# Optimization experiments

Measured on AMD Instinct MI355X. Metric: run time of the kernel, lower is better.

The kernel has to match this reference:

```python
import jax, jax.numpy as jnp
import numpy as np

B, LT, D, H, DI = 8, 128, 512, 8, 2048
NMEM, LMEM = 1024, 64
DH = D // H
EPS = 1e-5
NEG = -1e9

def _ln(x, g, b):
    mu = x.mean(-1, keepdims=True)
    var = ((x - mu) ** 2).mean(-1, keepdims=True)
    return (x - mu) * jax.lax.rsqrt(var + EPS) * g + b

def _ffn(x, W1, b1, W2, b2):
    # PositionwiseFF with residual=True (dropout=0 / eval)
    return x + jax.nn.relu(x @ W1 + b1) @ W2 + b2

def setup_inputs():
    key = jax.random.key(0)
    ks = jax.random.split(key, 16)
    w = lambda i, shape: jax.random.normal(ks[i], shape, jnp.float32) * 0.02
    return {
        "dec_output": jax.random.normal(ks[0], (B, LT, D), jnp.float32),
        "mem_attn_out": jax.random.normal(ks[1], (B, LT, NMEM + 1), jnp.float32),
        "enc_out_mem": jax.random.normal(ks[2], (NMEM, LMEM, D), jnp.float32),
        "tgt_emb_mem": jax.random.normal(ks[3], (NMEM, LMEM, D), jnp.float32),
        "tgt_mask_mem": jax.random.randint(ks[4], (NMEM, LMEM), 0, 2, jnp.int32),
        "tgt_mask": jax.random.randint(ks[5], (B, LT), 0, 2, jnp.int32),
        "g0": jnp.ones((D,), jnp.float32), "be0": jnp.zeros((D,), jnp.float32),
        "g1": jnp.ones((D,), jnp.float32), "be1": jnp.zeros((D,), jnp.float32),
        "Wq": w(6, (D, D)), "bq": jnp.zeros((D,), jnp.float32),
        "Wk": w(7, (D, D)), "bk": jnp.zeros((D,), jnp.float32),
        "Wv": w(8, (D, D)), "bv": jnp.zeros((D,), jnp.float32),
        "Wo": w(9, (D, D)), "bo": jnp.zeros((D,), jnp.float32),
        "f1W1": w(10, (D, DI)), "f1b1": jnp.zeros((DI,), jnp.float32),
        "f1W2": w(11, (DI, D)), "f1b2": jnp.zeros((D,), jnp.float32),
        "f2W1": w(12, (D, DI)), "f2b1": jnp.zeros((DI,), jnp.float32),
        "f2W2": w(13, (DI, D)), "f2b2": jnp.zeros((D,), jnp.float32),
    }

def reference(dec_output, mem_attn_out, enc_out_mem, tgt_emb_mem, tgt_mask_mem, tgt_mask,
              g0, be0, g1, be1, Wq, bq, Wk, bk, Wv, bv, Wo, bo,
              f1W1, f1b1, f1W2, f1b2, f2W1, f2b1, f2W2, f2b2):
    x = _ln(dec_output, g0, be0)                       # [B,LT,D]
    N = B * LT
    samples = jnp.argmax(mem_attn_out, -1).reshape(N) - 1   # [-1, NMEM-1]
    valid = samples >= 0                               # [N]
    s = jnp.maximum(samples, 0)                        # clamp; masked later
    q = x.reshape(N, 1, D)
    # gather memory per selected query (torch compacts via unique; same math)
    k_in = enc_out_mem[s]                              # [N,LMEM,D]
    v_in = tgt_emb_mem[s]                              # [N,LMEM,D]
    kmask = tgt_mask_mem[s] != 0                       # True = valid key
    # multi-head attention, residual=True
    qh = (q @ Wq + bq).reshape(N, 1, H, DH).transpose(0, 2, 1, 3)     # [N,H,1,DH]
    kh = (k_in @ Wk + bk).reshape(N, LMEM, H, DH).transpose(0, 2, 1, 3)
    vh = (v_in @ Wv + bv).reshape(N, LMEM, H, DH).transpose(0, 2, 1, 3)
    scores = jnp.einsum('nhqd,nhkd->nhqk', qh, kh) / (DH ** 0.5)      # [N,H,1,LMEM]
    scores = jnp.where(kmask[:, None, None, :], scores, NEG)
    attn = jax.nn.softmax(scores, axis=-1)
    ctx = jnp.einsum('nhqk,nhkd->nhqd', attn, vh).transpose(0, 2, 1, 3).reshape(N, 1, D)
    st = q + ctx @ Wo + bo
    st = _ffn(st, f1W1, f1b1, f1W2, f1b2)
    st = _ln(st, g1, be1)
    # scatter back: positions with sample == -1 get zeros
    st = jnp.where(valid[:, None, None], st, 0.0)
    dec = x + st.reshape(B, LT, D)
    dec = _ffn(dec, f2W1, f2b1, f2W2, f2b2)
    return dec
```

## Files before the change

kernel.cpp:

```cpp
#include <hip/hip_runtime.h>
#include <math.h>

#define NQ   1024
#define DIM  512
#define NH   8
#define DHD  64
#define DFF  2048
#define LM   64

typedef __bf16 bf16x8 __attribute__((ext_vector_type(8)));
typedef float  f32x4  __attribute__((ext_vector_type(4)));

__device__ __forceinline__ unsigned short f2bf(float f) {
    unsigned u = __builtin_bit_cast(unsigned, f);
    return (unsigned short)((u + 0x7fffu + ((u >> 16) & 1u)) >> 16);
}
__device__ __forceinline__ float bflo(unsigned p) {
    return __builtin_bit_cast(float, p << 16);
}
__device__ __forceinline__ float bfhi(unsigned p) {
    return __builtin_bit_cast(float, p & 0xffff0000u);
}

__device__ __forceinline__ void gload16(const void* g, void* l) {
    __builtin_amdgcn_global_load_lds(
        (const __attribute__((address_space(1))) unsigned*)g,
        (__attribute__((address_space(3))) unsigned*)l, 16, 0, 0);
}

__device__ __forceinline__ float blk_sum(float v, volatile float* red) {
#pragma unroll
    for (int o = 32; o; o >>= 1) v += __shfl_down(v, o);
    __syncthreads();
    if ((threadIdx.x & 63) == 0) red[threadIdx.x >> 6] = v;
    __syncthreads();
    return red[0] + red[1] + red[2] + red[3];
}

__global__ __launch_bounds__(256) void ln0_argmax_k(
    const float* __restrict__ dec_out, const float* __restrict__ attn_out,
    const float* __restrict__ g, const float* __restrict__ be,
    float* __restrict__ x, unsigned* __restrict__ xb, int* __restrict__ samples)
{
    __shared__ float red[4];
    __shared__ float rv[4]; __shared__ int ri[4];
    const int n = blockIdx.x, t = threadIdx.x;

    float2 v = ((const float2*)(dec_out + (size_t)n * DIM))[t];
    float mu  = blk_sum(v.x + v.y, red) * (1.f / DIM);
    float dx = v.x - mu, dy = v.y - mu;
    float var = blk_sum(dx * dx + dy * dy, red) * (1.f / DIM);
    float rs = rsqrtf(var + 1e-5f);
    float2 gg = ((const float2*)g)[t], bb = ((const float2*)be)[t];
    float ox = dx * rs * gg.x + bb.x, oy = dy * rs * gg.y + bb.y;
    ((float2*)(x + (size_t)n * DIM))[t] = make_float2(ox, oy);
    xb[(size_t)n * 256 + t] = (unsigned)f2bf(ox) | ((unsigned)f2bf(oy) << 16);

    const float* ar = attn_out + (size_t)n * 1025;
    float bv = -INFINITY; int bi = 0x7fffffff;
    for (int i = t; i < 1025; i += 256) {
        float val = ar[i];
        if (val > bv || (val == bv && i < bi)) { bv = val; bi = i; }
    }
#pragma unroll
    for (int o = 32; o; o >>= 1) {
        float ov = __shfl_down(bv, o); int oi = __shfl_down(bi, o);
        if (ov > bv || (ov == bv && oi < bi)) { bv = ov; bi = oi; }
    }
    if ((t & 63) == 0) { rv[t >> 6] = bv; ri[t >> 6] = bi; }
    __syncthreads();
    if (t == 0) {
#pragma unroll
        for (int w = 1; w < 4; ++w)
            if (rv[w] > bv || (rv[w] == bv && ri[w] < bi)) { bv = rv[w]; bi = ri[w]; }
        samples[n] = bi - 1;
    }
}

struct PrepPtrs {
    const float* src[8];
    unsigned short* dst[8];
};
__global__ __launch_bounds__(256) void prep_weights_k(PrepPtrs p) {
    __shared__ float tile[32][33];
    const int bid = blockIdx.x;
    int m, lt;
    if (bid < 1024) { m = bid >> 8; lt = bid & 255; }
    else { m = 4 + ((bid - 1024) >> 10); lt = (bid - 1024) & 1023; }
    const int RS = (m < 4) ? 512 : ((m == 5 || m == 7) ? 2048 : 512);
    const int CS = (m < 4) ? 512 : ((m == 5 || m == 7) ? 512 : 2048);
    const int TC = CS >> 5;
    const int tr = lt / TC, tc = lt % TC;
    const float* s = p.src[m];
    unsigned short* d = p.dst[m];
    const int tx = threadIdx.x & 31, ty = threadIdx.x >> 5;
    if (m == 1) {
#pragma unroll
        for (int i = 0; i < 32; i += 8) {
            size_t idx = (size_t)(tr * 32 + ty + i) * CS + tc * 32 + tx;
            d[idx] = f2bf(s[idx]);
        }
    } else {
#pragma unroll
        for (int i = 0; i < 32; i += 8)
            tile[ty + i][tx] = s[(size_t)(tr * 32 + ty + i) * CS + tc * 32 + tx];
        __syncthreads();
#pragma unroll
        for (int i = 0; i < 32; i += 8)
            d[(size_t)(tc * 32 + ty + i) * RS + tr * 32 + tx] = f2bf(tile[tx][ty + i]);
    }
}

template<bool RELU, bool BIAS, bool RES, bool WF32, bool WBF>
__global__ __launch_bounds__(256) void mfma_gemm(
    const unsigned short* __restrict__ A, const unsigned short* __restrict__ Bt,
    float* __restrict__ Cf, unsigned short* __restrict__ Cb,
    const float* __restrict__ bias, const float* __restrict__ res,
    int K, int lda, int ldb, int ldc,
    int sA, int sB, int sC, int sBias)
{
    __shared__ unsigned short Ab[2][64 * 64];
    __shared__ unsigned short Bb[2][64 * 64];
    const int t = threadIdx.x, lane = t & 63, wid = t >> 6;
    const int bm = blockIdx.y * 64, bn = blockIdx.x * 64, bz = blockIdx.z;
    const unsigned short* Abase = A + (size_t)bz * sA + (size_t)bm * lda;
    const unsigned short* Bbase = Bt + (size_t)bz * sB + (size_t)bn * ldb;

    const int r0 = wid * 16 + (lane >> 3);
    const int cbs = lane & 7;

#define STAGE_T(buf, base, ld, kt)                                              \
    {                                                                           \
        int r_ = r0;                                                            \
        gload16(base + (size_t)r_ * ld + (kt) * 64 + ((cbs ^ (r_ & 7)) << 3),   \
                &buf[(wid * 2 + 0) * 512]);                                     \
        r_ = r0 + 8;                                                            \
        gload16(base + (size_t)r_ * ld + (kt) * 64 + ((cbs ^ (r_ & 7)) << 3),   \
                &buf[(wid * 2 + 1) * 512]);                                     \
    }

    const int lr = lane & 15, lg = lane >> 4;
    const int wr = (wid >> 1) * 32, wc = (wid & 1) * 32;
    const int mA0 = wr + lr, mA1 = wr + 16 + lr;
    const int nB0 = wc + lr, nB1 = wc + 16 + lr;
    f32x4 acc[2][2] = {};

#define COMPUTE(b)                                                              \
    _Pragma("unroll")                                                           \
    for (int kk = 0; kk < 2; ++kk) {                                            \
        const int kb = kk * 4 + lg;                                             \
        bf16x8 a0 = *(const bf16x8*)&Ab[b][mA0 * 64 + ((kb ^ (mA0 & 7)) << 3)]; \
        bf16x8 a1 = *(const bf16x8*)&Ab[b][mA1 * 64 + ((kb ^ (mA1 & 7)) << 3)]; \
        bf16x8 b0 = *(const bf16x8*)&Bb[b][nB0 * 64 + ((kb ^ (nB0 & 7)) << 3)]; \
        bf16x8 b1 = *(const bf16x8*)&Bb[b][nB1 * 64 + ((kb ^ (nB1 & 7)) << 3)]; \
        acc[0][0] = __builtin_amdgcn_mfma_f32_16x16x32_bf16(a0, b0, acc[0][0], 0, 0, 0); \
        acc[0][1] = __builtin_amdgcn_mfma_f32_16x16x32_bf16(a0, b1, acc[0][1], 0, 0, 0); \
        acc[1][0] = __builtin_amdgcn_mfma_f32_16x16x32_bf16(a1, b0, acc[1][0], 0, 0, 0); \
        acc[1][1] = __builtin_amdgcn_mfma_f32_16x16x32_bf16(a1, b1, acc[1][1], 0, 0, 0); \
    }

    STAGE_T(Ab[0], Abase, lda, 0);
    STAGE_T(Bb[0], Bbase, ldb, 0);
    __syncthreads();
    const int NT = K >> 6;
    int cur = 0;
    for (int kt = 0; kt < NT; ++kt) {
        if (kt + 1 < NT) {
            STAGE_T(Ab[cur ^ 1], Abase, lda, kt + 1);
            STAGE_T(Bb[cur ^ 1], Bbase, ldb, kt + 1);
        }
        if (cur == 0) { COMPUTE(0); } else { COMPUTE(1); }
        __syncthreads();
        cur ^= 1;
    }

#pragma unroll
    for (int fm = 0; fm < 2; ++fm)
#pragma unroll
    for (int fn = 0; fn < 2; ++fn) {
        const int col = bn + wc + fn * 16 + lr;
        float bia = BIAS ? bias[bz * sBias + col] : 0.f;
#pragma unroll
        for (int r = 0; r < 4; ++r) {
            const int row = bm + wr + fm * 16 + lg * 4 + r;
            const size_t ci = (size_t)bz * sC + (size_t)row * ldc + col;
            float v = acc[fm][fn][r] + bia;
            if (RES) v += res[(size_t)row * ldc + col];
            if (RELU) v = fmaxf(v, 0.f);
            if (WF32) Cf[ci] = v;
            if (WBF)  Cb[ci] = f2bf(v);
        }
    }
#undef STAGE_T
#undef COMPUTE
}

__global__ __launch_bounds__(256) void attn_mem_k(
    const float* __restrict__ qh, const unsigned short* __restrict__ u_bf,
    const float* __restrict__ enc, const float* __restrict__ vemb,
    const int* __restrict__ maskmem, const int* __restrict__ samples,
    const float* __restrict__ bk, unsigned* __restrict__ a_bf)
{
    __shared__ alignas(16) unsigned short U_lds[16 * 512];
    __shared__ float S_lds[8 * 68];
    __shared__ alignas(16) unsigned short P_lds[64 * 8];
    __shared__ float Cs_lds[8];
    __shared__ int Msk_lds[64];

    const int n = blockIdx.x, t = threadIdx.x;
    const int lane = t & 63, w = t >> 6;
    int s = samples[n]; if (s < 0) s = 0;

    {
        const uint4* ub = (const uint4*)(u_bf + (size_t)n * 4096);
#pragma unroll
        for (int i = 0; i < 4; ++i) {
            int chunk = t + i * 256;
            int h = chunk >> 6, c8 = chunk & 63;
            uint4 v = (h < 8) ? ub[chunk] : make_uint4(0, 0, 0, 0);
            *(uint4*)&U_lds[h * 512 + (c8 ^ (h & 7)) * 8] = v;
        }
        if (w == 0) Msk_lds[lane] = maskmem[(size_t)s * LM + lane];
        if (w == 1) {
            int h = lane >> 3, j = lane & 7;
            const float4* q4 = (const float4*)(qh + (size_t)n * DIM + h * 64 + j * 8);
            const float4* b4 = (const float4*)(bk + h * 64 + j * 8);
            float4 qa = q4[0], qb = q4[1], ba = b4[0], bb = b4[1];
            float c = qa.x * ba.x + qa.y * ba.y + qa.z * ba.z + qa.w * ba.w
                    + qb.x * bb.x + qb.y * bb.y + qb.z * bb.z + qb.w * bb.w;
            c += __shfl_xor(c, 1); c += __shfl_xor(c, 2); c += __shfl_xor(c, 4);
            if (j == 0) Cs_lds[h] = c;
        }
    }
    __syncthreads();

    {
        const float4* kb = (const float4*)(enc + (size_t)s * (LM * DIM));
        const int key = w * 16 + (lane & 15);
        const int lg = lane >> 4;
        const int h = lane & 15;
        const int base = key * 128 + lg * 2;
        f32x4 acc = {};
        float4 pf[4][2];
#pragma unroll
        for (int ss = 0; ss < 4; ++ss) {
            pf[ss][0] = kb[base + ss * 8];
            pf[ss][1] = kb[base + ss * 8 + 1];
        }
#pragma unroll
        for (int step = 0; step < 16; ++step) {
            float4 a0 = pf[step & 3][0], a1 = pf[step & 3][1];
            if (step + 4 < 16) {
                pf[step & 3][0] = kb[base + (step + 4) * 8];
                pf[step & 3][1] = kb[base + (step + 4) * 8 + 1];
            }
            bf16x8 af;
            af[0] = (__bf16)a0.x; af[1] = (__bf16)a0.y;
            af[2] = (__bf16)a0.z; af[3] = (__bf16)a0.w;
            af[4] = (__bf16)a1.x; af[5] = (__bf16)a1.y;
            af[6] = (__bf16)a1.z; af[7] = (__bf16)a1.w;
            const int c8 = step * 4 + lg;
            bf16x8 bfr = *(const bf16x8*)&U_lds[h * 512 + (c8 ^ (h & 7)) * 8];
            acc = __builtin_amdgcn_mfma_f32_16x16x32_bf16(af, bfr, acc, 0, 0, 0);
        }
        if (h < 8) {
#pragma unroll
            for (int r = 0; r < 4; ++r)
                S_lds[h * 68 + w * 16 + lg * 4 + r] = acc[r];
        }
    }
    __syncthreads();

#pragma unroll
    for (int hh = 0; hh < 2; ++hh) {
        const int h = w + hh * 4;
        float sc = (S_lds[h * 68 + lane] + Cs_lds[h]) * 0.125f;
        sc = (Msk_lds[lane] != 0) ? sc : -1e9f;
        float m = sc;
#pragma unroll
        for (int o = 32; o; o >>= 1) m = fmaxf(m, __shfl_xor(m, o));
        float e = __expf(sc - m);
        float su = e;
#pragma unroll
        for (int o = 32; o; o >>= 1) su += __shfl_xor(su, o);
        P_lds[lane * 8 + h] = f2bf(e / su);
    }
    __syncthreads();

    {
        float2 acc8[8];
#pragma unroll
        for (int h = 0; h < 8; ++h) acc8[h] = make_float2(0.f, 0.f);
        const float2* vb = (const float2*)(vemb + (size_t)s * (LM * DIM)) + t;
#pragma unroll 8
        for (int k = 0; k < 64; ++k) {
            float2 v = vb[k * 256];
            uint4 pr = *(const uint4*)&P_lds[k * 8];
            float p0 = bflo(pr.x), p1 = bfhi(pr.x);
            float p2 = bflo(pr.y), p3 = bfhi(pr.y);
            float p4 = bflo(pr.z), p5 = bfhi(pr.z);
            float p6 = bflo(pr.w), p7 = bfhi(pr.w);
            acc8[0].x = fmaf(p0, v.x, acc8[0].x); acc8[0].y = fmaf(p0, v.y, acc8[0].y);
            acc8[1].x = fmaf(p1, v.x, acc8[1].x); acc8[1].y = fmaf(p1, v.y, acc8[1].y);
            acc8[2].x = fmaf(p2, v.x, acc8[2].x); acc8[2].y = fmaf(p2, v.y, acc8[2].y);
            acc8[3].x = fmaf(p3, v.x, acc8[3].x); acc8[3].y = fmaf(p3, v.y, acc8[3].y);
            acc8[4].x = fmaf(p4, v.x, acc8[4].x); acc8[4].y = fmaf(p4, v.y, acc8[4].y);
            acc8[5].x = fmaf(p5, v.x, acc8[5].x); acc8[5].y = fmaf(p5, v.y, acc8[5].y);
            acc8[6].x = fmaf(p6, v.x, acc8[6].x); acc8[6].y = fmaf(p6, v.y, acc8[6].y);
            acc8[7].x = fmaf(p7, v.x, acc8[7].x); acc8[7].y = fmaf(p7, v.y, acc8[7].y);
        }
        unsigned* an = a_bf + (size_t)n * 2048;
#pragma unroll
        for (int h = 0; h < 8; ++h)
            an[h * 256 + t] = (unsigned)f2bf(acc8[h].x) | ((unsigned)f2bf(acc8[h].y) << 16);
    }
}

__global__ __launch_bounds__(256) void ln1_mask_add_k(
    const float* __restrict__ t1, const float* __restrict__ g,
    const float* __restrict__ be, const int* __restrict__ samples,
    const float* __restrict__ x, float* __restrict__ dec, unsigned* __restrict__ decb)
{
    __shared__ float red[4];
    const int n = blockIdx.x, t = threadIdx.x;
    float2 v = ((const float2*)(t1 + (size_t)n * DIM))[t];
    float mu  = blk_sum(v.x + v.y, red) * (1.f / DIM);
    float dx = v.x - mu, dy = v.y - mu;
    float var = blk_sum(dx * dx + dy * dy, red) * (1.f / DIM);
    float rs = rsqrtf(var + 1e-5f);
    float2 gg = ((const float2*)g)[t], bb = ((const float2*)be)[t];
    float sx = dx * rs * gg.x + bb.x, sy = dy * rs * gg.y + bb.y;
    if (samples[n] < 0) { sx = 0.f; sy = 0.f; }
    float2 xx = ((const float2*)(x + (size_t)n * DIM))[t];
    float ox = xx.x + sx, oy = xx.y + sy;
    ((float2*)(dec + (size_t)n * DIM))[t] = make_float2(ox, oy);
    decb[(size_t)n * 256 + t] = (unsigned)f2bf(ox) | ((unsigned)f2bf(oy) << 16);
}

extern "C" void kernel_launch(void* const* d_in, const int* in_sizes, int n_in,
                              void* d_out, int out_size, void* d_ws, size_t ws_size,
                              hipStream_t stream)
{
    const float* dec_output = (const float*)d_in[0];
    const float* mem_attn   = (const float*)d_in[1];
    const float* enc_mem    = (const float*)d_in[2];
    const float* temb_mem   = (const float*)d_in[3];
    const int*   mask_mem   = (const int*)d_in[4];
    const float* g0  = (const float*)d_in[6];
    const float* be0 = (const float*)d_in[7];
    const float* g1  = (const float*)d_in[8];
    const float* be1 = (const float*)d_in[9];
    const float* Wq  = (const float*)d_in[10];
    const float* bq  = (const float*)d_in[11];
    const float* Wk  = (const float*)d_in[12];
    const float* bk  = (const float*)d_in[13];
    const float* Wv  = (const float*)d_in[14];
    const float* bv  = (const float*)d_in[15];
    const float* Wo  = (const float*)d_in[16];
    const float* bo  = (const float*)d_in[17];
    const float* f1W1 = (const float*)d_in[18];
    const float* f1b1 = (const float*)d_in[19];
    const float* f1W2 = (const float*)d_in[20];
    const float* f1b2 = (const float*)d_in[21];
    const float* f2W1 = (const float*)d_in[22];
    const float* f2b1 = (const float*)d_in[23];
    const float* f2W2 = (const float*)d_in[24];
    const float* f2b2 = (const float*)d_in[25];
    float* out = (float*)d_out;

    float* ws = (float*)d_ws;
    float*          x_f   = ws + 0;
    unsigned*       x_b   = (unsigned*)(ws + 524288);
    float*          qh_f  = ws + 786432;
    unsigned short* qh_b  = (unsigned short*)(ws + 1310720);
    unsigned short* u_b   = (unsigned short*)(ws + 1572864);
    unsigned short* a_b   = (unsigned short*)(ws + 3670016);
    unsigned short* wqt   = (unsigned short*)(ws + 5767168);
    unsigned short* wkc   = (unsigned short*)(ws + 5898240);
    unsigned short* wvt   = (unsigned short*)(ws + 6029312);
    unsigned short* wot   = (unsigned short*)(ws + 6160384);
    unsigned short* f1w1t = (unsigned short*)(ws + 6291456);
    unsigned short* f1w2t = (unsigned short*)(ws + 6815744);
    unsigned short* f2w1t = (unsigned short*)(ws + 7340032);
    unsigned short* f2w2t = (unsigned short*)(ws + 7864320);
    int*            smp   = (int*)(ws + 8388608);
    float*          st0_f = (float*)u_b + 0;
    unsigned short* st0_b = (unsigned short*)((float*)u_b + 524288);
    float*          t1_f  = (float*)u_b + 786432;
    float*          dec_f = (float*)u_b + 1310720;
    unsigned*       dec_b = (unsigned*)((float*)u_b + 1835008);
    unsigned short* h1_b  = a_b;
    unsigned short* h2_b  = (unsigned short*)((float*)a_b + 1048576);

    PrepPtrs pp;
    pp.src[0] = Wq;   pp.dst[0] = wqt;
    pp.src[1] = Wk;   pp.dst[1] = wkc;
    pp.src[2] = Wv;   pp.dst[2] = wvt;
    pp.src[3] = Wo;   pp.dst[3] = wot;
    pp.src[4] = f1W1; pp.dst[4] = f1w1t;
    pp.src[5] = f1W2; pp.dst[5] = f1w2t;
    pp.src[6] = f2W1; pp.dst[6] = f2w1t;
    pp.src[7] = f2W2; pp.dst[7] = f2w2t;
    prep_weights_k<<<5120, 256, 0, stream>>>(pp);
    ln0_argmax_k<<<NQ, 256, 0, stream>>>(dec_output, mem_attn, g0, be0, x_f, x_b, smp);
    mfma_gemm<false, true, false, true, true><<<dim3(8, 16, 1), 256, 0, stream>>>(
        (const unsigned short*)x_b, wqt, qh_f, qh_b, bq, nullptr,
        DIM, DIM, DIM, DIM, 0, 0, 0, 0);
    mfma_gemm<false, false, false, false, true><<<dim3(8, 16, NH), 256, 0, stream>>>(
        qh_b, wkc, nullptr, u_b, nullptr, nullptr,
        DHD, DIM, DIM, NH * DIM, DHD, DHD, DIM, 0);
    attn_mem_k<<<NQ, 256, 0, stream>>>(qh_f, u_b, enc_mem, temb_mem, mask_mem, smp,
                                       bk, (unsigned*)a_b);
    mfma_gemm<false, true, false, false, true><<<dim3(1, 16, NH), 256, 0, stream>>>(
        a_b, wvt, nullptr, qh_b, bv, nullptr,
        DIM, NH * DIM, DIM, DIM, DIM, DHD * DIM, DHD, DHD);
    mfma_gemm<false, true, true, true, true><<<dim3(8, 16, 1), 256, 0, stream>>>(
        qh_b, wot, st0_f, st0_b, bo, x_f, DIM, DIM, DIM, DIM, 0, 0, 0, 0);
    mfma_gemm<true, true, false, false, true><<<dim3(32, 16, 1), 256, 0, stream>>>(
        st0_b, f1w1t, nullptr, h1_b, f1b1, nullptr, DIM, DIM, DIM, DFF, 0, 0, 0, 0);
    mfma_gemm<false, true, true, true, false><<<dim3(8, 16, 1), 256, 0, stream>>>(
        h1_b, f1w2t, t1_f, nullptr, f1b2, st0_f, DFF, DFF, DFF, DIM, 0, 0, 0, 0);
    ln1_mask_add_k<<<NQ, 256, 0, stream>>>(t1_f, g1, be1, smp, x_f, dec_f, dec_b);
    mfma_gemm<true, true, false, false, true><<<dim3(32, 16, 1), 256, 0, stream>>>(
        (const unsigned short*)dec_b, f2w1t, nullptr, h2_b, f2b1, nullptr,
        DIM, DIM, DIM, DFF, 0, 0, 0, 0);
    mfma_gemm<false, true, true, true, false><<<dim3(8, 16, 1), 256, 0, stream>>>(
        h2_b, f2w2t, out, nullptr, f2b2, dec_f, DFF, DFF, DFF, DIM, 0, 0, 0, 0);

    (void)in_sizes; (void)n_in; (void)out_size; (void)ws_size;
}
```

Baseline: 162.7 us.

## Split memory attention into scores and PV kernels; add 128x128 FFN up-projection GEMM

The fused memory-attention kernel is split into a scores/softmax kernel and a separate P·V kernel. The scores kernel reads the projected query fragments straight from global memory instead of staging them in LDS. The P·V kernel runs two blocks per query, each covering half the columns, with the key range split across half-blocks and reduced through LDS, which doubles parallelism. A new double-buffered 128x128-tile MFMA GEMM replaces the generic GEMM for both FFN first layers, raising per-block data reuse at the cost of fewer blocks (128) and more registers.

Measured after the change: 172.7 us. +6.2%, slower.

```diff
diff --git a/kernel.cpp b/kernel.cpp
--- a/kernel.cpp
+++ b/kernel.cpp
@@ -195,15 +195,98 @@
 #undef COMPUTE
 }
 
-__global__ __launch_bounds__(256) void attn_mem_k(
+template<bool RELU>
+__global__ __launch_bounds__(256) void mfma_gemm128(
+    const unsigned short* __restrict__ A, const unsigned short* __restrict__ Bt,
+    unsigned short* __restrict__ Cb, const float* __restrict__ bias,
+    int K, int lda, int ldb, int ldc)
+{
+    __shared__ unsigned short Ab[2][128 * 64];
+    __shared__ unsigned short Bb[2][128 * 64];
+    const int t = threadIdx.x, lane = t & 63, wid = t >> 6;
+    const int bn = blockIdx.x * 128, bm = blockIdx.y * 128;
+    const unsigned short* Abase = A + (size_t)bm * lda;
+    const unsigned short* Bbase = Bt + (size_t)bn * ldb;
+
+    const int srow = lane >> 3;
+    const int c8 = lane & 7;
+
+#define STAGE128(buf, base, ld, kt)                                             \
+    _Pragma("unroll")                                                           \
+    for (int i = 0; i < 4; ++i) {                                               \
+        int row = i * 32 + wid * 8 + srow;                                      \
+        gload16(base + (size_t)row * ld + (kt) * 64 + ((c8 ^ (row & 7)) << 3),  \
+                &buf[(i * 32 + wid * 8) * 64]);                                 \
+    }
+
+    const int lr = lane & 15, lg = lane >> 4;
+    const int wr = (wid >> 1) * 64, wc = (wid & 1) * 64;
+    f32x4 acc[4][4] = {};
+
+#define COMPUTE128(b)                                                           \
+    _Pragma("unroll")                                                           \
+    for (int kk = 0; kk < 2; ++kk) {                                            \
+        const int kb = kk * 4 + lg;                                             \
+        bf16x8 af[4], bfv[4];                                                   \
+        _Pragma("unroll")                                                       \
+        for (int fm = 0; fm < 4; ++fm) {                                        \
+            int row = wr + fm * 16 + lr;                                        \
+            af[fm] = *(const bf16x8*)&Ab[b][row * 64 + ((kb ^ (row & 7)) << 3)];\
+        }                                                                       \
+        _Pragma("unroll")                                                       \
+        for (int fn = 0; fn < 4; ++fn) {                                        \
+            int col = wc + fn * 16 + lr;                                        \
+            bfv[fn] = *(const bf16x8*)&Bb[b][col * 64 + ((kb ^ (col & 7)) << 3)];\
+        }                                                                       \
+        _Pragma("unroll")                                                       \
+        for (int fm = 0; fm < 4; ++fm)                                          \
+            _Pragma("unroll")                                                   \
+            for (int fn = 0; fn < 4; ++fn)                                      \
+                acc[fm][fn] = __builtin_amdgcn_mfma_f32_16x16x32_bf16(          \
+                    af[fm], bfv[fn], acc[fm][fn], 0, 0, 0);                     \
+    }
+
+    STAGE128(Ab[0], Abase, lda, 0);
+    STAGE128(Bb[0], Bbase, ldb, 0);
+    __syncthreads();
+    const int NT = K >> 6;
+    int cur = 0;
+    for (int kt = 0; kt < NT; ++kt) {
+        if (kt + 1 < NT) {
+            STAGE128(Ab[cur ^ 1], Abase, lda, kt + 1);
+            STAGE128(Bb[cur ^ 1], Bbase, ldb, kt + 1);
+        }
+        if (cur == 0) { COMPUTE128(0); } else { COMPUTE128(1); }
+        __syncthreads();
+        cur ^= 1;
+    }
+
+#pragma unroll
+    for (int fn = 0; fn < 4; ++fn) {
+        const int col = bn + wc + fn * 16 + lr;
+        const float bia = bias[col];
+#pragma unroll
+        for (int fm = 0; fm < 4; ++fm) {
+#pragma unroll
+            for (int r = 0; r < 4; ++r) {
+                const int row = bm + wr + fm * 16 + lg * 4 + r;
+                float v = acc[fm][fn][r] + bia;
+                if (RELU) v = fmaxf(v, 0.f);
+                Cb[(size_t)row * ldc + col] = f2bf(v);
+            }
+        }
+    }
+#undef STAGE128
+#undef COMPUTE128
+}
+
+__global__ __launch_bounds__(256) void attn_scores_k(
     const float* __restrict__ qh, const unsigned short* __restrict__ u_bf,
-    const float* __restrict__ enc, const float* __restrict__ vemb,
-    const int* __restrict__ maskmem, const int* __restrict__ samples,
-    const float* __restrict__ bk, unsigned* __restrict__ a_bf)
-{
-    __shared__ alignas(16) unsigned short U_lds[16 * 512];
+    const float* __restrict__ enc, const int* __restrict__ maskmem,
+    const int* __restrict__ samples, const float* __restrict__ bk,
+    unsigned short* __restrict__ p_out)
+{
     __shared__ float S_lds[8 * 68];
-    __shared__ alignas(16) unsigned short P_lds[64 * 8];
     __shared__ float Cs_lds[8];
     __shared__ int Msk_lds[64];
 
@@ -211,70 +294,59 @@
     const int lane = t & 63, w = t >> 6;
     int s = samples[n]; if (s < 0) s = 0;
 
-    {
-        const uint4* ub = (const uint4*)(u_bf + (size_t)n * 4096);
-#pragma unroll
-        for (int i = 0; i < 4; ++i) {
-            int chunk = t + i * 256;
-            int h = chunk >> 6, c8 = chunk & 63;
-            uint4 v = (h < 8) ? ub[chunk] : make_uint4(0, 0, 0, 0);
-            *(uint4*)&U_lds[h * 512 + (c8 ^ (h & 7)) * 8] = v;
-        }
-        if (w == 0) Msk_lds[lane] = maskmem[(size_t)s * LM + lane];
-        if (w == 1) {
-            int h = lane >> 3, j = lane & 7;
-            const float4* q4 = (const float4*)(qh + (size_t)n * DIM + h * 64 + j * 8);
-            const float4* b4 = (const float4*)(bk + h * 64 + j * 8);
-            float4 qa = q4[0], qb = q4[1], ba = b4[0], bb = b4[1];
-            float c = qa.x * ba.x + qa.y * ba.y + qa.z * ba.z + qa.w * ba.w
-                    + qb.x * bb.x + qb.y * bb.y + qb.z * bb.z + qb.w * bb.w;
-            c += __shfl_xor(c, 1); c += __shfl_xor(c, 2); c += __shfl_xor(c, 4);
-            if (j == 0) Cs_lds[h] = c;
-        }
-    }
-    __syncthreads();
-
-    {
-        const float4* kb = (const float4*)(enc + (size_t)s * (LM * DIM));
-        const int key = w * 16 + (lane & 15);
-        const int lg = lane >> 4;
-        const int h = lane & 15;
-        const int base = key * 128 + lg * 2;
-        f32x4 acc = {};
-        float4 pf[4][2];
-#pragma unroll
-        for (int ss = 0; ss < 4; ++ss) {
-            pf[ss][0] = kb[base + ss * 8];
-            pf[ss][1] = kb[base + ss * 8 + 1];
-        }
-#pragma unroll
-        for (int step = 0; step < 16; ++step) {
-            float4 a0 = pf[step & 3][0], a1 = pf[step & 3][1];
-            if (step + 4 < 16) {
-                pf[step & 3][0] = kb[base + (step + 4) * 8];
-                pf[step & 3][1] = kb[base + (step + 4) * 8 + 1];
-            }
-            bf16x8 af;
-            af[0] = (__bf16)a0.x; af[1] = (__bf16)a0.y;
-            af[2] = (__bf16)a0.z; af[3] = (__bf16)a0.w;
-            af[4] = (__bf16)a1.x; af[5] = (__bf16)a1.y;
-            af[6] = (__bf16)a1.z; af[7] = (__bf16)a1.w;
-            const int c8 = step * 4 + lg;
-            bf16x8 bfr = *(const bf16x8*)&U_lds[h * 512 + (c8 ^ (h & 7)) * 8];
-            acc = __builtin_amdgcn_mfma_f32_16x16x32_bf16(af, bfr, acc, 0, 0, 0);
-        }
-        if (h < 8) {
-#pragma unroll
-            for (int r = 0; r < 4; ++r)
-                S_lds[h * 68 + w * 16 + lg * 4 + r] = acc[r];
-        }
-    }
-    __syncthreads();
-
+    const float4* kb = (const float4*)(enc + (size_t)s * (LM * DIM));
+    const int key = w * 16 + (lane & 15);
+    const int lg = lane >> 4;
+    const int h = lane & 15;
+    const int base = key * 128 + lg * 2;
+    float4 pf[4][2];
+#pragma unroll
+    for (int ss = 0; ss < 4; ++ss) {
+        pf[ss][0] = kb[base + ss * 8];
+        pf[ss][1] = kb[base + ss * 8 + 1];
+    }
+
+    if (w == 0) Msk_lds[lane] = maskmem[(size_t)s * LM + lane];
+    if (w == 1) {
+        int hq = lane >> 3, j = lane & 7;
+        const float4* q4 = (const float4*)(qh + (size_t)n * DIM + hq * 64 + j * 8);
+        const float4* b4 = (const float4*)(bk + hq * 64 + j * 8);
+        float4 qa = q4[0], qb = q4[1], ba = b4[0], bb = b4[1];
+        float c = qa.x * ba.x + qa.y * ba.y + qa.z * ba.z + qa.w * ba.w
+                + qb.x * bb.x + qb.y * bb.y + qb.z * bb.z + qb.w * bb.w;
+        c += __shfl_xor(c, 1); c += __shfl_xor(c, 2); c += __shfl_xor(c, 4);
+        if (j == 0) Cs_lds[hq] = c;
+    }
+
+    const unsigned short* ub = u_bf + (size_t)n * 4096 + (size_t)(h & 7) * 512;
+    f32x4 acc = {};
+#pragma unroll
+    for (int step = 0; step < 16; ++step) {
+        float4 a0 = pf[step & 3][0], a1 = pf[step & 3][1];
+        if (step + 4 < 16) {
+            pf[step & 3][0] = kb[base + (step + 4) * 8];
+            pf[step & 3][1] = kb[base + (step + 4) * 8 + 1];
+        }
+        bf16x8 af;
+        af[0] = (__bf16)a0.x; af[1] = (__bf16)a0.y;
+        af[2] = (__bf16)a0.z; af[3] = (__bf16)a0.w;
+        af[4] = (__bf16)a1.x; af[5] = (__bf16)a1.y;
+        af[6] = (__bf16)a1.z; af[7] = (__bf16)a1.w;
+        bf16x8 bfr = *(const bf16x8*)&ub[(step * 4 + lg) * 8];
+        acc = __builtin_amdgcn_mfma_f32_16x16x32_bf16(af, bfr, acc, 0, 0, 0);
+    }
+    if (h < 8) {
+#pragma unroll
+        for (int r = 0; r < 4; ++r)
+            S_lds[h * 68 + w * 16 + lg * 4 + r] = acc[r];
+    }
+    __syncthreads();
+
+    unsigned short* pg = p_out + (size_t)n * 512 + lane * 8;
 #pragma unroll
     for (int hh = 0; hh < 2; ++hh) {
-        const int h = w + hh * 4;
-        float sc = (S_lds[h * 68 + lane] + Cs_lds[h]) * 0.125f;
+        const int h2 = w + hh * 4;
+        float sc = (S_lds[h2 * 68 + lane] + Cs_lds[h2]) * 0.125f;
         sc = (Msk_lds[lane] != 0) ? sc : -1e9f;
         float m = sc;
 #pragma unroll
@@ -283,36 +355,58 @@
         float su = e;
 #pragma unroll
         for (int o = 32; o; o >>= 1) su += __shfl_xor(su, o);
-        P_lds[lane * 8 + h] = f2bf(e / su);
-    }
-    __syncthreads();
-
-    {
-        float2 acc8[8];
-#pragma unroll
-        for (int h = 0; h < 8; ++h) acc8[h] = make_float2(0.f, 0.f);
-        const float2* vb = (const float2*)(vemb + (size_t)s * (LM * DIM)) + t;
+        pg[h2] = f2bf(e / su);
+    }
+}
+
+__global__ __launch_bounds__(256) void attn_pv_k(
+    const unsigned short* __restrict__ p_in, const float* __restrict__ vemb,
+    const int* __restrict__ samples, unsigned* __restrict__ a_bf)
+{
+    __shared__ uint4 P_lds[64];
+    __shared__ float2 Red[8][128];
+    const int n = blockIdx.x, dh = blockIdx.y, t = threadIdx.x;
+    int s = samples[n]; if (s < 0) s = 0;
+
+    if (t < 64) P_lds[t] = ((const uint4*)(p_in + (size_t)n * 512))[t];
+    __syncthreads();
+
+    const int c = t & 127, kh = t >> 7;
+    const float2* vb = (const float2*)(vemb + (size_t)s * (LM * DIM)) + dh * 128 + c;
+    float2 acc8[8];
+#pragma unroll
+    for (int hh = 0; hh < 8; ++hh) acc8[hh] = make_float2(0.f, 0.f);
 #pragma unroll 8
-        for (int k = 0; k < 64; ++k) {
-            float2 v = vb[k * 256];
-            uint4 pr = *(const uint4*)&P_lds[k * 8];
-            float p0 = bflo(pr.x), p1 = bfhi(pr.x);
-            float p2 = bflo(pr.y), p3 = bfhi(pr.y);
-            float p4 = bflo(pr.z), p5 = bfhi(pr.z);
-            float p6 = bflo(pr.w), p7 = bfhi(pr.w);
-            acc8[0].x = fmaf(p0, v.x, acc8[0].x); acc8[0].y = fmaf(p0, v.y, acc8[0].y);
-            acc8[1].x = fmaf(p1, v.x, acc8[1].x); acc8[1].y = fmaf(p1, v.y, acc8[1].y);
-            acc8[2].x = fmaf(p2, v.x, acc8[2].x); acc8[2].y = fmaf(p2, v.y, acc8[2].y);
-            acc8[3].x = fmaf(p3, v.x, acc8[3].x); acc8[3].y = fmaf(p3, v.y, acc8[3].y);
-            acc8[4].x = fmaf(p4, v.x, acc8[4].x); acc8[4].y = fmaf(p4, v.y, acc8[4].y);
-            acc8[5].x = fmaf(p5, v.x, acc8[5].x); acc8[5].y = fmaf(p5, v.y, acc8[5].y);
-            acc8[6].x = fmaf(p6, v.x, acc8[6].x); acc8[6].y = fmaf(p6, v.y, acc8[6].y);
-            acc8[7].x = fmaf(p7, v.x, acc8[7].x); acc8[7].y = fmaf(p7, v.y, acc8[7].y);
-        }
-        unsigned* an = a_bf + (size_t)n * 2048;
-#pragma unroll
-        for (int h = 0; h < 8; ++h)
-            an[h * 256 + t] = (unsigned)f2bf(acc8[h].x) | ((unsigned)f2bf(acc8[h].y) << 16);
+    for (int i = 0; i < 32; ++i) {
+        const int k = kh * 32 + i;
+        float2 v = vb[(size_t)k * 256];
+        uint4 pr = P_lds[k];
+        float p0 = bflo(pr.x), p1 = bfhi(pr.x);
+        float p2 = bflo(pr.y), p3 = bfhi(pr.y);
+        float p4 = bflo(pr.z), p5 = bfhi(pr.z);
+        float p6 = bflo(pr.w), p7 = bfhi(pr.w);
+        acc8[0].x = fmaf(p0, v.x, acc8[0].x); acc8[0].y = fmaf(p0, v.y, acc8[0].y);
+        acc8[1].x = fmaf(p1, v.x, acc8[1].x); acc8[1].y = fmaf(p1, v.y, acc8[1].y);
+        acc8[2].x = fmaf(p2, v.x, acc8[2].x); acc8[2].y = fmaf(p2, v.y, acc8[2].y);
+        acc8[3].x = fmaf(p3, v.x, acc8[3].x); acc8[3].y = fmaf(p3, v.y, acc8[3].y);
+        acc8[4].x = fmaf(p4, v.x, acc8[4].x); acc8[4].y = fmaf(p4, v.y, acc8[4].y);
+        acc8[5].x = fmaf(p5, v.x, acc8[5].x); acc8[5].y = fmaf(p5, v.y, acc8[5].y);
+        acc8[6].x = fmaf(p6, v.x, acc8[6].x); acc8[6].y = fmaf(p6, v.y, acc8[6].y);
+        acc8[7].x = fmaf(p7, v.x, acc8[7].x); acc8[7].y = fmaf(p7, v.y, acc8[7].y);
+    }
+    if (kh == 1) {
+#pragma unroll
+        for (int hh = 0; hh < 8; ++hh) Red[hh][c] = acc8[hh];
+    }
+    __syncthreads();
+    if (kh == 0) {
+        unsigned* an = a_bf + (size_t)n * 2048 + dh * 128;
+#pragma unroll
+        for (int hh = 0; hh < 8; ++hh) {
+            float2 r = Red[hh][c];
+            float ox = acc8[hh].x + r.x, oy = acc8[hh].y + r.y;
+            an[hh * 256 + c] = (unsigned)f2bf(ox) | ((unsigned)f2bf(oy) << 16);
+        }
     }
 }
 
@@ -384,6 +478,7 @@
     unsigned short* f2w1t = (unsigned short*)(ws + 7340032);
     unsigned short* f2w2t = (unsigned short*)(ws + 7864320);
     int*            smp   = (int*)(ws + 8388608);
+    unsigned short* p_b   = (unsigned short*)x_b;
     float*          st0_f = (float*)u_b + 0;
     unsigned short* st0_b = (unsigned short*)((float*)u_b + 524288);
     float*          t1_f  = (float*)u_b + 786432;
@@ -409,21 +504,20 @@
     mfma_gemm<false, false, false, false, true><<<dim3(8, 16, NH), 256, 0, stream>>>(
         qh_b, wkc, nullptr, u_b, nullptr, nullptr,
         DHD, DIM, DIM, NH * DIM, DHD, DHD, DIM, 0);
-    attn_mem_k<<<NQ, 256, 0, stream>>>(qh_f, u_b, enc_mem, temb_mem, mask_mem, smp,
-                                       bk, (unsigned*)a_b);
+    attn_scores_k<<<NQ, 256, 0, stream>>>(qh_f, u_b, enc_mem, mask_mem, smp, bk, p_b);
+    attn_pv_k<<<dim3(NQ, 2), 256, 0, stream>>>(p_b, temb_mem, smp, (unsigned*)a_b);
     mfma_gemm<false, true, false, false, true><<<dim3(1, 16, NH), 256, 0, stream>>>(
         a_b, wvt, nullptr, qh_b, bv, nullptr,
         DIM, NH * DIM, DIM, DIM, DIM, DHD * DIM, DHD, DHD);
     mfma_gemm<false, true, true, true, true><<<dim3(8, 16, 1), 256, 0, stream>>>(
         qh_b, wot, st0_f, st0_b, bo, x_f, DIM, DIM, DIM, DIM, 0, 0, 0, 0);
-    mfma_gemm<true, true, false, false, true><<<dim3(32, 16, 1), 256, 0, stream>>>(
-        st0_b, f1w1t, nullptr, h1_b, f1b1, nullptr, DIM, DIM, DIM, DFF, 0, 0, 0, 0);
+    mfma_gemm128<true><<<dim3(16, 8), 256, 0, stream>>>(
+        st0_b, f1w1t, h1_b, f1b1, DIM, DIM, DIM, DFF);
     mfma_gemm<false, true, true, true, false><<<dim3(8, 16, 1), 256, 0, stream>>>(
         h1_b, f1w2t, t1_f, nullptr, f1b2, st0_f, DFF, DFF, DFF, DIM, 0, 0, 0, 0);
     ln1_mask_add_k<<<NQ, 256, 0, stream>>>(t1_f, g1, be1, smp, x_f, dec_f, dec_b);
-    mfma_gemm<true, true, false, false, true><<<dim3(32, 16, 1), 256, 0, stream>>>(
-        (const unsigned short*)dec_b, f2w1t, nullptr, h2_b, f2b1, nullptr,
-        DIM, DIM, DIM, DFF, 0, 0, 0, 0);
+    mfma_gemm128<true><<<dim3(16, 8), 256, 0, stream>>>(
+        (const unsigned short*)dec_b, f2w1t, h2_b, f2b1, DIM, DIM, DIM, DFF);
     mfma_gemm<false, true, true, true, false><<<dim3(8, 16, 1), 256, 0, stream>>>(
         h2_b, f2w2t, out, nullptr, f2b2, dec_f, DFF, DFF, DFF, DIM, 0, 0, 0, 0);
 
```
